# Optimization experiments

Hardware: AMD Instinct MI355X
Metric: run time of the kernel (lower is better)

Reference implementation:

```python
import jax, jax.numpy as jnp
import numpy as np

B, IN, N, OUT = 65536, 512, 256, 64  # batch, in_size, neurons, out_size


def setup_inputs() -> dict:
    key = jax.random.key(0)
    k1, k2, k3, k4 = jax.random.split(key, 4)
    return {
        "x": jax.random.normal(k1, (B, IN), jnp.float32),
        "W_lin": jax.random.normal(k2, (IN, N + OUT), jnp.float32),   # nlinear
        "W_nl": jax.random.normal(k3, (N - 1, N), jnp.float32),        # padded nonlinear[i] rows
        "W_out": jax.random.normal(k4, (OUT, N), jnp.float32),         # output_weights[0:out_size]
    }


def reference(x, W_lin, W_nl, W_out):
    act = jnp.tanh
    lin = x @ W_lin  # [B, N+OUT]
    # row i of nonlinear weights is valid only for entries 0..i (length i+1)
    tri_mask = (jnp.arange(N)[None, :] <= jnp.arange(N - 1)[:, None]).astype(lin.dtype)
    Wm = W_nl * tri_mask  # [N-1, N]
    # growing accumulator, fixed-size buffer; position 0 = lin[0] + 1
    acc0 = jnp.zeros((x.shape[0], N), lin.dtype).at[:, 0].set(lin[:, 0] + 1.0)
    col = jnp.arange(N)[None, :]

    def step(acc, inp):
        w, l, i = inp  # w: [N] masked weights, l: [B] = lin[:, i], i: scalar step
        v = jnp.sum(act(acc) * w[None, :], axis=1) + l + 1.0  # [B]
        acc = jnp.where(col == (i + 1), v[:, None], acc)
        return acc, None

    xs = (Wm, lin[:, : N - 1].T, jnp.arange(N - 1))
    acc, _ = jax.lax.scan(step, acc0, xs)
    # outs[i] = act(t) @ output_weights[i] + lin[neurons + i] + 1
    out = act(acc) @ W_out.T + lin[:, N:] + 1.0  # [B, OUT]
    return out
```

## Files before the change

kernel.cpp:

```cpp
#include <hip/hip_runtime.h>
#include <hip/hip_bf16.h>

typedef _Float16 f16x8 __attribute__((ext_vector_type(8)));
typedef unsigned short u16x8 __attribute__((ext_vector_type(8)));
typedef float f32x4 __attribute__((ext_vector_type(4)));
typedef unsigned int u32x4 __attribute__((ext_vector_type(4)));

static __device__ __forceinline__ unsigned short h2u(_Float16 h) {
    return __builtin_bit_cast(unsigned short, h);
}
static __device__ __forceinline__ float fast_tanh(float x) {
    float e = __expf(2.0f * x);
    return 1.0f - 2.0f / (e + 1.0f);
}

__global__ void cascade_prep(const float* __restrict__ W_lin,
                             const float* __restrict__ W_nl,
                             const float* __restrict__ W_out,
                             unsigned short* __restrict__ wlin_h,
                             unsigned short* __restrict__ wlin_l,
                             unsigned short* __restrict__ wnl_h,
                             unsigned short* __restrict__ wnl_l,
                             unsigned short* __restrict__ wout_h,
                             unsigned short* __restrict__ wout_l,
                             float* __restrict__ wcol) {
    int idx = blockIdx.x * blockDim.x + threadIdx.x;
    int stride = gridDim.x * blockDim.x;
    for (int i = idx; i < 320 * 512; i += stride) {
        int n = i >> 9, k = i & 511;
        float w = W_lin[k * 320 + n];
        _Float16 h = (_Float16)w;
        wlin_h[i] = h2u(h);
        wlin_l[i] = h2u((_Float16)(w - (float)h));
    }
    for (int i = idx; i < 255 * 256; i += stride) {
        int r = i >> 8, k = i & 255;
        float w = (k <= r) ? W_nl[i] : 0.0f;
        _Float16 h = (_Float16)w;
        wnl_h[i] = h2u(h);
        wnl_l[i] = h2u((_Float16)(w - (float)h));
    }
    for (int i = idx; i < 64 * 256; i += stride) {
        float w = W_out[i];
        _Float16 h = (_Float16)w;
        wout_h[i] = h2u(h);
        wout_l[i] = h2u((_Float16)(w - (float)h));
    }
    for (int i = idx; i < 256; i += stride) {
        int b = i >> 5, u = i & 31;
        float* dst = wcol + b * 496 + (31 * u - (u * (u - 1)) / 2);
        for (int j = u + 1; j < 32; ++j)
            dst[j - u - 1] = W_nl[(size_t)(b * 32 + j - 1) * 256 + b * 32 + u];
    }
}

__global__ __launch_bounds__(512, 1) void lin_gemm(
    const float* __restrict__ x,
    const unsigned short* __restrict__ wlin_h,
    const unsigned short* __restrict__ wlin_l,
    float* __restrict__ linc,
    float* __restrict__ lino) {

    __shared__ _Float16 bufH[2][16 * 520];
    __shared__ _Float16 bufL[2][16 * 520];

    const int tid = threadIdx.x;
    const int wv  = tid >> 6;
    const int l15 = tid & 15;
    const int g   = (tid & 63) >> 4;
    const int s = (blockIdx.x & 7) * 64 + (blockIdx.x >> 3);
    const long row0 = (long)s * 128;

    f16x8 xfh[16], xfl[16];
    {
        const float* xp = x + (row0 + wv * 16 + l15) * 512 + g * 8;
        #pragma unroll
        for (int ks = 0; ks < 16; ++ks) {
            float4 p0 = *reinterpret_cast<const float4*>(xp + ks * 32);
            float4 p1 = *reinterpret_cast<const float4*>(xp + ks * 32 + 4);
            float av[8] = {p0.x, p0.y, p0.z, p0.w, p1.x, p1.y, p1.z, p1.w};
            f16x8 fh, fl;
            #pragma unroll
            for (int e = 0; e < 8; ++e) {
                _Float16 hh = (_Float16)av[e];
                fh[e] = hh;
                fl[e] = (_Float16)(av[e] - (float)hh);
            }
            xfh[ks] = fh;
            xfl[ks] = fl;
        }
    }

    u16x8 rh[2], rl[2];
    #define STAGE_LOAD(nt)                                                     \
        {                                                                      \
            _Pragma("unroll")                                                  \
            for (int it = 0; it < 2; ++it) {                                   \
                int flat = it * 4096 + tid * 8;                                \
                int r = flat >> 9, c = flat & 511;                             \
                rh[it] = *reinterpret_cast<const u16x8*>(                      \
                    wlin_h + (size_t)((nt) * 16 + r) * 512 + c);               \
                rl[it] = *reinterpret_cast<const u16x8*>(                      \
                    wlin_l + (size_t)((nt) * 16 + r) * 512 + c);               \
            }                                                                  \
        }
    #define STAGE_WRITE(buf)                                                   \
        {                                                                      \
            _Pragma("unroll")                                                  \
            for (int it = 0; it < 2; ++it) {                                   \
                int flat = it * 4096 + tid * 8;                                \
                int r = flat >> 9, c = flat & 511;                             \
                *reinterpret_cast<u16x8*>(&bufH[buf][r * 520 + c]) =           \
                    __builtin_bit_cast(u16x8, rh[it]);                         \
                *reinterpret_cast<u16x8*>(&bufL[buf][r * 520 + c]) =           \
                    __builtin_bit_cast(u16x8, rl[it]);                         \
            }                                                                  \
        }

    STAGE_LOAD(0);
    STAGE_WRITE(0);
    __syncthreads();

    int cur = 0;
    for (int nt = 0; nt < 20; ++nt) {
        if (nt < 19) STAGE_LOAD(nt + 1);

        f32x4 acc = (f32x4){0.f, 0.f, 0.f, 0.f};
        if (nt < 16) {
            #pragma unroll
            for (int ks = 0; ks < 16; ++ks) {
                f16x8 bh = *reinterpret_cast<const f16x8*>(
                    &bufH[cur][l15 * 520 + ks * 32 + g * 8]);
                f16x8 bl = *reinterpret_cast<const f16x8*>(
                    &bufL[cur][l15 * 520 + ks * 32 + g * 8]);
                acc = __builtin_amdgcn_mfma_f32_16x16x32_f16(xfh[ks], bh, acc, 0, 0, 0);
                acc = __builtin_amdgcn_mfma_f32_16x16x32_f16(xfl[ks], bh, acc, 0, 0, 0);
                acc = __builtin_amdgcn_mfma_f32_16x16x32_f16(xfh[ks], bl, acc, 0, 0, 0);
            }
            int c = nt * 16 + l15;
            #pragma unroll
            for (int j = 0; j < 4; ++j) {
                long row = row0 + wv * 16 + g * 4 + j;
                if (c < 255) linc[row * 256 + c + 1] = acc[j];
                if (c == 0)  linc[row * 256] = acc[j];
            }
        } else {
            #pragma unroll
            for (int ks = 0; ks < 16; ++ks) {
                f16x8 bh = *reinterpret_cast<const f16x8*>(
                    &bufH[cur][l15 * 520 + ks * 32 + g * 8]);
                acc = __builtin_amdgcn_mfma_f32_16x16x32_f16(xfh[ks], bh, acc, 0, 0, 0);
            }
            #pragma unroll
            for (int j = 0; j < 4; ++j)
                lino[(row0 + wv * 16 + g * 4 + j) * 64 + (nt - 16) * 16 + l15] = acc[j];
        }

        if (nt < 19) STAGE_WRITE(cur ^ 1);
        __syncthreads();
        cur ^= 1;
    }
    #undef STAGE_LOAD
    #undef STAGE_WRITE
}

static __device__ __forceinline__ void unpack_pf(u32x4 a0, u32x4 a1,
                                                 f16x8* ah, f16x8* al) {
    u32x4 hx, lx;
    hx[0] = (a0[0] & 0xffffu) | (a0[1] << 16);
    hx[1] = (a0[2] & 0xffffu) | (a0[3] << 16);
    hx[2] = (a1[0] & 0xffffu) | (a1[1] << 16);
    hx[3] = (a1[2] & 0xffffu) | (a1[3] << 16);
    lx[0] = (a0[0] >> 16) | (a0[1] & 0xffff0000u);
    lx[1] = (a0[2] >> 16) | (a0[3] & 0xffff0000u);
    lx[2] = (a1[0] >> 16) | (a1[1] & 0xffff0000u);
    lx[3] = (a1[2] >> 16) | (a1[3] & 0xffff0000u);
    *ah = __builtin_bit_cast(f16x8, hx);
    *al = __builtin_bit_cast(f16x8, lx);
}

__global__ __launch_bounds__(64) void cascade_casc(
    const float* __restrict__ linc,
    const float* __restrict__ lino,
    const float* __restrict__ wcol,
    const unsigned short* __restrict__ wnl_h,
    const unsigned short* __restrict__ wnl_l,
    const unsigned short* __restrict__ wout_h,
    const unsigned short* __restrict__ wout_l,
    float* __restrict__ out) {

    __shared__ float conacc[16 * 260];
    __shared__ float wslab[500];

    const int l   = threadIdx.x;
    const int l15 = l & 15;
    const int g   = l >> 4;
    const int s = (blockIdx.x & 7) * 512 + (blockIdx.x >> 3);
    const long row0 = (long)s * 16;

    unsigned int* conp = reinterpret_cast<unsigned int*>(conacc);

    #pragma unroll
    for (int it = 0; it < 16; ++it) {
        int flat = it * 256 + l * 4;
        int rr = flat >> 8, c4 = flat & 255;
        float4 v = *reinterpret_cast<const float4*>(linc + (row0 + rr) * 256 + c4);
        *reinterpret_cast<float4*>(&conacc[rr * 260 + c4]) = v;
    }
    __syncthreads();

    for (int b = 0; b < 8; ++b) {
        {
            int i0 = l * 4;
            float4 v0 = *reinterpret_cast<const float4*>(wcol + b * 496 + i0);
            *reinterpret_cast<float4*>(&wslab[i0]) = v0;
            int i1 = 256 + l * 4;
            if (i1 < 496) {
                float4 v1 = *reinterpret_cast<const float4*>(wcol + b * 496 + i1);
                *reinterpret_cast<float4*>(&wslab[i1]) = v1;
            }
        }
        __syncthreads();

        float acc[32];
        #pragma unroll
        for (int j = 0; j < 32; ++j) acc[j] = 0.0f;
        #pragma unroll
        for (int u8 = 0; u8 < 4; ++u8) {
            float4 cw0 = *reinterpret_cast<const float4*>(&conacc[l15 * 260 + b * 32 + u8 * 8]);
            float4 cw1 = *reinterpret_cast<const float4*>(&conacc[l15 * 260 + b * 32 + u8 * 8 + 4]);
            float conw[8] = {cw0.x, cw0.y, cw0.z, cw0.w, cw1.x, cw1.y, cw1.z, cw1.w};
            unsigned int pk[8];
            #pragma unroll
            for (int v = 0; v < 8; ++v) {
                const int u = u8 * 8 + v;
                float vv = acc[u] + conw[v] + 1.0f;
                float tv = fast_tanh(vv);
                _Float16 hv = (_Float16)tv;
                _Float16 lo = (_Float16)(tv - (float)hv);
                pk[v] = (unsigned int)h2u(hv) | ((unsigned int)h2u(lo) << 16);
                const float* wu = wslab + (31 * u - (u * (u - 1)) / 2);
                #pragma unroll
                for (int j = u + 1; j < 32; ++j)
                    acc[j] = fmaf(tv, wu[j - u - 1], acc[j]);
            }
            if (l < 16) {
                *reinterpret_cast<u32x4*>(&conp[l15 * 260 + b * 32 + u8 * 8]) =
                    (u32x4){pk[0], pk[1], pk[2], pk[3]};
                *reinterpret_cast<u32x4*>(&conp[l15 * 260 + b * 32 + u8 * 8 + 4]) =
                    (u32x4){pk[4], pk[5], pk[6], pk[7]};
            }
        }
        __syncthreads();

        if (b < 7) {
            f16x8 ah, al;
            {
                const unsigned int* p = &conp[l15 * 260 + b * 32 + g * 8];
                unpack_pf(*reinterpret_cast<const u32x4*>(p),
                          *reinterpret_cast<const u32x4*>(p + 4), &ah, &al);
            }
            for (int nt = 2 * (b + 1); nt < 16; ++nt) {
                const size_t wrow = (size_t)(nt * 16 + l15 - 1) * 256 + b * 32 + g * 8;
                f16x8 bh = __builtin_bit_cast(f16x8, *reinterpret_cast<const u16x8*>(wnl_h + wrow));
                f16x8 bl = __builtin_bit_cast(f16x8, *reinterpret_cast<const u16x8*>(wnl_l + wrow));
                f32x4 d = (f32x4){0.f, 0.f, 0.f, 0.f};
                d = __builtin_amdgcn_mfma_f32_16x16x32_f16(ah, bh, d, 0, 0, 0);
                d = __builtin_amdgcn_mfma_f32_16x16x32_f16(al, bh, d, 0, 0, 0);
                d = __builtin_amdgcn_mfma_f32_16x16x32_f16(ah, bl, d, 0, 0, 0);
                #pragma unroll
                for (int jj = 0; jj < 4; ++jj) {
                    int idx = (g * 4 + jj) * 260 + nt * 16 + l15;
                    conacc[idx] += d[jj];
                }
            }
        }
        __syncthreads();
    }

    #pragma unroll
    for (int n = 0; n < 4; ++n) {
        f32x4 acc = (f32x4){0.f, 0.f, 0.f, 0.f};
        #pragma unroll
        for (int kc = 0; kc < 8; ++kc) {
            const unsigned int* p = &conp[l15 * 260 + kc * 32 + g * 8];
            f16x8 ah, al;
            unpack_pf(*reinterpret_cast<const u32x4*>(p),
                      *reinterpret_cast<const u32x4*>(p + 4), &ah, &al);
            const size_t wrow = (size_t)(n * 16 + l15) * 256 + kc * 32 + g * 8;
            f16x8 bh = __builtin_bit_cast(f16x8, *reinterpret_cast<const u16x8*>(wout_h + wrow));
            f16x8 bl = __builtin_bit_cast(f16x8, *reinterpret_cast<const u16x8*>(wout_l + wrow));
            acc = __builtin_amdgcn_mfma_f32_16x16x32_f16(ah, bh, acc, 0, 0, 0);
            acc = __builtin_amdgcn_mfma_f32_16x16x32_f16(al, bh, acc, 0, 0, 0);
            acc = __builtin_amdgcn_mfma_f32_16x16x32_f16(ah, bl, acc, 0, 0, 0);
        }
        #pragma unroll
        for (int j = 0; j < 4; ++j) {
            long rr = row0 + g * 4 + j;
            int c = n * 16 + l15;
            out[rr * 64 + c] = acc[j] + lino[rr * 64 + c] + 1.0f;
        }
    }
}

extern "C" void kernel_launch(void* const* d_in, const int* in_sizes, int n_in,
                              void* d_out, int out_size, void* d_ws, size_t ws_size,
                              hipStream_t stream) {
    (void)in_sizes; (void)n_in; (void)out_size; (void)ws_size;
    const float* x     = (const float*)d_in[0];
    const float* W_lin = (const float*)d_in[1];
    const float* W_nl  = (const float*)d_in[2];
    const float* W_out = (const float*)d_in[3];
    float* out = (float*)d_out;

    char* ws = (char*)d_ws;
    unsigned short* wlin_h = (unsigned short*)(ws);
    unsigned short* wlin_l = (unsigned short*)(ws + 327680);
    unsigned short* wnl_h  = (unsigned short*)(ws + 916480);
    unsigned short* wnl_l  = (unsigned short*)(ws + 1047040);
    unsigned short* wout_h = (unsigned short*)(ws + 1177600);
    unsigned short* wout_l = (unsigned short*)(ws + 1210368);
    float*          wcol   = (float*)(ws + 1243136);
    float*          linc   = (float*)(ws + 1259008);
    float*          lino   = (float*)(ws + 68367872);

    cascade_prep<<<256, 256, 0, stream>>>(W_lin, W_nl, W_out,
                                          wlin_h, wlin_l, wnl_h, wnl_l,
                                          wout_h, wout_l, wcol);
    lin_gemm<<<512, 512, 0, stream>>>(x, wlin_h, wlin_l, linc, lino);
    cascade_casc<<<4096, 64, 0, stream>>>(linc, lino, wcol,
                                          wnl_h, wnl_l, wout_h, wout_l, out);
}
```

Baseline: 238.2 us.

## Defer cascade MFMA updates into next block's serial tanh loop

The MFMA update of later column tiles from block b is moved into iteration b+1. The two tiles needed immediately are updated before the barrier. The remaining tiles are interleaved with the serial scalar tanh/FMA chain, so matrix-core work overlaps VALU work, and one __syncthreads per block iteration is removed. The block loop is also fully unrolled, which raises register pressure and code size. Correctness depends on the later tiles not being read before their deferred update.

```diff
diff --git a/kernel.cpp b/kernel.cpp
--- a/kernel.cpp
+++ b/kernel.cpp
@@ -191,14 +191,13 @@
 
     __shared__ float conacc[16 * 260];
     __shared__ float wslab[500];
+    unsigned int* conp = reinterpret_cast<unsigned int*>(conacc);
 
     const int l   = threadIdx.x;
     const int l15 = l & 15;
     const int g   = l >> 4;
     const int s = (blockIdx.x & 7) * 512 + (blockIdx.x >> 3);
     const long row0 = (long)s * 16;
-
-    unsigned int* conp = reinterpret_cast<unsigned int*>(conacc);
 
     #pragma unroll
     for (int it = 0; it < 16; ++it) {
@@ -209,6 +208,26 @@
     }
     __syncthreads();
 
+    #define NT_UPDATE(bs, nt, AH, AL)                                          \
+        {                                                                      \
+            const size_t wrow = (size_t)((nt) * 16 + l15 - 1) * 256            \
+                                + (bs) * 32 + g * 8;                           \
+            f16x8 bh_ = __builtin_bit_cast(f16x8,                              \
+                *reinterpret_cast<const u16x8*>(wnl_h + wrow));                \
+            f16x8 bl_ = __builtin_bit_cast(f16x8,                              \
+                *reinterpret_cast<const u16x8*>(wnl_l + wrow));                \
+            f32x4 d_ = (f32x4){0.f, 0.f, 0.f, 0.f};                            \
+            d_ = __builtin_amdgcn_mfma_f32_16x16x32_f16(AH, bh_, d_, 0, 0, 0); \
+            d_ = __builtin_amdgcn_mfma_f32_16x16x32_f16(AL, bh_, d_, 0, 0, 0); \
+            d_ = __builtin_amdgcn_mfma_f32_16x16x32_f16(AH, bl_, d_, 0, 0, 0); \
+            _Pragma("unroll")                                                  \
+            for (int jj_ = 0; jj_ < 4; ++jj_) {                                \
+                int idx_ = (g * 4 + jj_) * 260 + (nt) * 16 + l15;              \
+                conacc[idx_] += d_[jj_];                                       \
+            }                                                                  \
+        }
+
+    #pragma unroll
     for (int b = 0; b < 8; ++b) {
         {
             int i0 = l * 4;
@@ -220,6 +239,14 @@
                 *reinterpret_cast<float4*>(&wslab[i1]) = v1;
             }
         }
+        f16x8 pah = {}, pal = {};
+        if (b >= 1) {
+            const unsigned int* p = &conp[l15 * 260 + (b - 1) * 32 + g * 8];
+            unpack_pf(*reinterpret_cast<const u32x4*>(p),
+                      *reinterpret_cast<const u32x4*>(p + 4), &pah, &pal);
+            NT_UPDATE(b - 1, 2 * b, pah, pal);
+            NT_UPDATE(b - 1, 2 * b + 1, pah, pal);
+        }
         __syncthreads();
 
         float acc[32];
@@ -230,6 +257,15 @@
             float4 cw0 = *reinterpret_cast<const float4*>(&conacc[l15 * 260 + b * 32 + u8 * 8]);
             float4 cw1 = *reinterpret_cast<const float4*>(&conacc[l15 * 260 + b * 32 + u8 * 8 + 4]);
             float conw[8] = {cw0.x, cw0.y, cw0.z, cw0.w, cw1.x, cw1.y, cw1.z, cw1.w};
+
+            if (b >= 1) {
+                #pragma unroll
+                for (int q = 0; q < 3; ++q) {
+                    const int nt = 2 * b + 2 + u8 * 3 + q;
+                    if (nt < 16) NT_UPDATE(b - 1, nt, pah, pal);
+                }
+            }
+
             unsigned int pk[8];
             #pragma unroll
             for (int v = 0; v < 8; ++v) {
@@ -252,31 +288,8 @@
             }
         }
         __syncthreads();
-
-        if (b < 7) {
-            f16x8 ah, al;
-            {
-                const unsigned int* p = &conp[l15 * 260 + b * 32 + g * 8];
-                unpack_pf(*reinterpret_cast<const u32x4*>(p),
-                          *reinterpret_cast<const u32x4*>(p + 4), &ah, &al);
-            }
-            for (int nt = 2 * (b + 1); nt < 16; ++nt) {
-                const size_t wrow = (size_t)(nt * 16 + l15 - 1) * 256 + b * 32 + g * 8;
-                f16x8 bh = __builtin_bit_cast(f16x8, *reinterpret_cast<const u16x8*>(wnl_h + wrow));
-                f16x8 bl = __builtin_bit_cast(f16x8, *reinterpret_cast<const u16x8*>(wnl_l + wrow));
-                f32x4 d = (f32x4){0.f, 0.f, 0.f, 0.f};
-                d = __builtin_amdgcn_mfma_f32_16x16x32_f16(ah, bh, d, 0, 0, 0);
-                d = __builtin_amdgcn_mfma_f32_16x16x32_f16(al, bh, d, 0, 0, 0);
-                d = __builtin_amdgcn_mfma_f32_16x16x32_f16(ah, bl, d, 0, 0, 0);
-                #pragma unroll
-                for (int jj = 0; jj < 4; ++jj) {
-                    int idx = (g * 4 + jj) * 260 + nt * 16 + l15;
-                    conacc[idx] += d[jj];
-                }
-            }
-        }
-        __syncthreads();
-    }
+    }
+    #undef NT_UPDATE
 
     #pragma unroll
     for (int n = 0; n < 4; ++n) {
```

After: 232.3 us. -2.5%, faster.
